# Kernel tuning notes

Hardware: AMD Instinct MI355X
Metric: run time of the kernel (lower is better)

The kernel has to match this reference:

```python
import jax, jax.numpy as jnp
import numpy as np

D_MODEL = 1024
N_HEADS = 16
D_K = 64
B = 2
S = 2048


def setup_inputs() -> dict:
    key = jax.random.key(0)
    ks = jax.random.split(key, 6)
    scale = 1.0 / np.sqrt(D_MODEL)
    x = jax.random.normal(ks[0], (B, S, D_MODEL), dtype=jnp.float32)
    Wq = jax.random.normal(ks[1], (D_MODEL, D_MODEL), dtype=jnp.float32) * scale
    Wk = jax.random.normal(ks[2], (D_MODEL, D_MODEL), dtype=jnp.float32) * scale
    Wv = jax.random.normal(ks[3], (D_MODEL, D_MODEL), dtype=jnp.float32) * scale
    Wo = jax.random.normal(ks[4], (D_MODEL, D_MODEL), dtype=jnp.float32) * scale
    bq = jnp.zeros((D_MODEL,), jnp.float32)
    bk = jnp.zeros((D_MODEL,), jnp.float32)
    bv = jnp.zeros((D_MODEL,), jnp.float32)
    bo = jnp.zeros((D_MODEL,), jnp.float32)
    # causal mask, broadcast over batch and heads: [1, 1, S, S]
    mask = jnp.tril(jnp.ones((S, S), jnp.int32))[None, None, :, :]
    return {"x": x, "mask": mask, "Wq": Wq, "bq": bq, "Wk": Wk, "bk": bk,
            "Wv": Wv, "bv": bv, "Wo": Wo, "bo": bo}


def reference(x, mask, Wq, bq, Wk, bk, Wv, bv, Wo, bo):
    b, s, _ = x.shape
    # projections (torch Linear: y = x @ W^T + b); split heads -> [b, h, s, d_k]
    def split_heads(y):
        return y.reshape(b, s, N_HEADS, D_K).transpose(0, 2, 1, 3)
    Q = split_heads(x @ Wq.T + bq)
    K = split_heads(x @ Wk.T + bk)
    V = split_heads(x @ Wv.T + bv)
    scores = jnp.einsum('bhqd,bhkd->bhqk', Q, K) / jnp.sqrt(jnp.float32(D_K))
    scores = jnp.where(mask == 0, -jnp.inf, scores)
    attn = jax.nn.softmax(scores, axis=-1)  # dropout p=0 -> identity
    out = jnp.einsum('bhqk,bhkd->bhqd', attn, V)
    out = out.transpose(0, 2, 1, 3).reshape(b, s, D_MODEL)
    return out @ Wo.T + bo
```

## Files before the change

### kernel.cpp

```cpp
#include <hip/hip_runtime.h>
#include <math.h>
#include <type_traits>

#define D_MODEL 1024
#define N_HEADS 16
#define D_KK    64
#define B_SZ    2
#define SEQ     2048
#define M_TOTAL (B_SZ * SEQ)

#define QSCALE 0.18033688011112042f
#define FIXM 12.0f

typedef __attribute__((ext_vector_type(8)))  short short8;
typedef __attribute__((ext_vector_type(4)))  float f32x4;
typedef __attribute__((ext_vector_type(16))) float f32x16;

static __device__ __forceinline__ ushort f2bf(float f) {
    union { float f; unsigned u; } c; c.f = f;
    unsigned u = c.u;
    unsigned r = (u + 0x7fffu + ((u >> 16) & 1u)) >> 16;
    return (ushort)r;
}

static __device__ __forceinline__ unsigned cvtpk(float a, float b) {
    unsigned r;
    asm("v_cvt_pk_bf16_f32 %0, %1, %2" : "=v"(r) : "v"(a), "v"(b));
    return r;
}
static __device__ __forceinline__ void pswap(unsigned &a, unsigned &b) {
    asm("v_permlane32_swap_b32 %0, %1" : "+v"(a), "+v"(b));
}

static __device__ __forceinline__ void gload16(const void* g, void* l) {
    __builtin_amdgcn_global_load_lds(
        (const __attribute__((address_space(1))) void*)g,
        (__attribute__((address_space(3))) void*)l, 16, 0, 0);
}

__global__ __launch_bounds__(256)
void cvt_kernel(const float* __restrict__ x,  const float* __restrict__ wq,
                const float* __restrict__ wk, const float* __restrict__ wv,
                const float* __restrict__ wo,
                ushort* __restrict__ xb,  ushort* __restrict__ wqb,
                ushort* __restrict__ wkb, ushort* __restrict__ wvb,
                ushort* __restrict__ wob)
{
    const float* s; ushort* d; int n4;
    switch (blockIdx.y) {
        case 0:  s = x;  d = xb;  n4 = M_TOTAL * D_MODEL / 4; break;
        case 1:  s = wq; d = wqb; n4 = D_MODEL * D_MODEL / 4; break;
        case 2:  s = wk; d = wkb; n4 = D_MODEL * D_MODEL / 4; break;
        case 3:  s = wv; d = wvb; n4 = D_MODEL * D_MODEL / 4; break;
        default: s = wo; d = wob; n4 = D_MODEL * D_MODEL / 4; break;
    }
    const int stride = gridDim.x * blockDim.x;
    for (int i = blockIdx.x * blockDim.x + threadIdx.x; i < n4; i += stride) {
        float4 v = reinterpret_cast<const float4*>(s)[i];
        ushort4 u;
        u.x = f2bf(v.x); u.y = f2bf(v.y); u.z = f2bf(v.z); u.w = f2bf(v.w);
        reinterpret_cast<ushort4*>(d)[i] = u;
    }
}

template<int EPI>
__global__ __launch_bounds__(256)
void gemm_mfma(const ushort* __restrict__ A,
               const ushort* __restrict__ W0, const float* __restrict__ b0, void* __restrict__ C0,
               const ushort* __restrict__ W1, const float* __restrict__ b1, void* __restrict__ C1,
               const ushort* __restrict__ W2, const float* __restrict__ b2, void* __restrict__ C2)
{
    constexpr int K = D_MODEL;

    __shared__ ushort As[2][128 * 64];
    __shared__ ushort Bs[2][64 * 64];

    const int id  = blockIdx.x;
    const int xcd = id & 7;
    const int j   = id >> 3;
    const int mt  = xcd * 4 + (j & 3);
    const int ntz = j >> 2;
    const int nt  = ntz & 15;
    const int z   = ntz >> 4;

    const ushort* W    = W0;
    const float*  bias = b0;
    void*         C    = C0;
    if (z == 1) { W = W1; bias = b1; C = C1; }
    else if (z == 2) { W = W2; bias = b2; C = C2; }

    const int m0 = mt * 128;
    const int n0 = nt * 64;

    const int tid  = threadIdx.x;
    const int w    = tid >> 6;
    const int lane = tid & 63;
    const int lr   = lane & 15;
    const int lc   = lane >> 4;
    const int wr   = w >> 1;
    const int wc   = w & 1;

    const int rsub = lane >> 3;
    const int csw  = ((lane & 7) ^ rsub) << 3;

    const ushort* gA = A + (size_t)(m0 + w * 8 + rsub) * K + csw;
    const ushort* gB = W + (size_t)(n0 + w * 8 + rsub) * K + csw;

    f32x4 acc[4][2];
#pragma unroll
    for (int m = 0; m < 4; ++m)
#pragma unroll
        for (int n = 0; n < 2; ++n) acc[m][n] = (f32x4)0.0f;

#pragma unroll
    for (int ca = 0; ca < 4; ++ca)
        gload16(gA + (size_t)(32 * ca) * K, &As[0][(w + 4 * ca) * 512]);
#pragma unroll
    for (int cb = 0; cb < 2; ++cb)
        gload16(gB + (size_t)(32 * cb) * K, &Bs[0][(w + 4 * cb) * 512]);
    __syncthreads();

    const int swz = (lr & 7) << 4;
    int buf = 0;
    for (int it = 0; it < 16; ++it) {
        if (it < 15) {
            const int kn = (it + 1) * 64;
#pragma unroll
            for (int ca = 0; ca < 4; ++ca)
                gload16(gA + (size_t)(32 * ca) * K + kn, &As[buf ^ 1][(w + 4 * ca) * 512]);
#pragma unroll
            for (int cb = 0; cb < 2; ++cb)
                gload16(gB + (size_t)(32 * cb) * K + kn, &Bs[buf ^ 1][(w + 4 * cb) * 512]);
        }

        short8 af[4][2], bfr[2][2];
#pragma unroll
        for (int m = 0; m < 4; ++m) {
            const int rbyte = (wr * 64 + m * 16 + lr) * 128;
#pragma unroll
            for (int kk = 0; kk < 2; ++kk)
                af[m][kk] = *reinterpret_cast<const short8*>(
                    &As[buf][(rbyte + ((kk * 64 + lc * 16) ^ swz)) >> 1]);
        }
#pragma unroll
        for (int n = 0; n < 2; ++n) {
            const int rbyte = (wc * 32 + n * 16 + lr) * 128;
#pragma unroll
            for (int kk = 0; kk < 2; ++kk)
                bfr[n][kk] = *reinterpret_cast<const short8*>(
                    &Bs[buf][(rbyte + ((kk * 64 + lc * 16) ^ swz)) >> 1]);
        }
#pragma unroll
        for (int kk = 0; kk < 2; ++kk)
#pragma unroll
            for (int m = 0; m < 4; ++m)
#pragma unroll
                for (int n = 0; n < 2; ++n)
                    acc[m][n] = __builtin_amdgcn_mfma_f32_16x16x32_bf16(
                        af[m][kk], bfr[n][kk], acc[m][n], 0, 0, 0);

        __syncthreads();
        buf ^= 1;
    }

    float bv[2];
#pragma unroll
    for (int n = 0; n < 2; ++n) bv[n] = bias[n0 + wc * 32 + n * 16 + lr];
    const int row_base = m0 + wr * 64;

    if (EPI == 0) {
        float* Cf = (float*)C;
#pragma unroll
        for (int m = 0; m < 4; ++m)
#pragma unroll
        for (int r = 0; r < 4; ++r) {
            const int row = row_base + m * 16 + lc * 4 + r;
#pragma unroll
            for (int n = 0; n < 2; ++n)
                Cf[(size_t)row * D_MODEL + n0 + wc * 32 + n * 16 + lr] =
                    acc[m][n][r] + bv[n];
        }
    } else {
        ushort* Cu = (ushort*)C;
        const bool vt   = (z == 2);
        const float osc = (z == 0) ? QSCALE : 1.0f;
#pragma unroll
        for (int m = 0; m < 4; ++m) {
            const int row4 = row_base + m * 16 + lc * 4;
            const int bb = row4 >> 11;
            const int ss = row4 & 2047;
            const size_t bhbase = (size_t)bb * N_HEADS;
#pragma unroll
            for (int n = 0; n < 2; ++n) {
                const int col = n0 + wc * 32 + n * 16 + lr;
                const int h = col >> 6, d = col & 63;
                if (vt) {
                    ushort4 u;
                    u.x = f2bf(acc[m][n][0] + bv[n]);
                    u.y = f2bf(acc[m][n][1] + bv[n]);
                    u.z = f2bf(acc[m][n][2] + bv[n]);
                    u.w = f2bf(acc[m][n][3] + bv[n]);
                    *reinterpret_cast<ushort4*>(
                        &Cu[((bhbase + h) * D_KK + d) * SEQ + ss]) = u;
                } else {
#pragma unroll
                    for (int r = 0; r < 4; ++r)
                        Cu[((bhbase + h) * SEQ + ss + r) * D_KK + d] =
                            f2bf((acc[m][n][r] + bv[n]) * osc);
                }
            }
        }
    }
}

__global__ __launch_bounds__(128)
void attn_mfma_kernel(const ushort* __restrict__ Qb, const ushort* __restrict__ Kb,
                      const ushort* __restrict__ Vt, ushort* __restrict__ Ob)
{
    __shared__ ushort Ks[2][4096];
    __shared__ ushort Vs[2][4096];

    const int tid  = threadIdx.x;
    const int w    = tid >> 6;
    const int lane = tid & 63;
    const int l31  = lane & 31;
    const int hi   = lane >> 5;
    const int swl  = (lane & 7) << 4;

    const int id  = blockIdx.x;
    const int xcd = id & 7;
    const int j   = id >> 3;
    const int bh  = xcd * 4 + (j & 3);
    const int qx  = j >> 2;
    const int b   = bh >> 4;
    const int h   = bh & 15;

    const ushort* Kbase = Kb + (size_t)bh * SEQ * D_KK;
    const ushort* Vbase = Vt + (size_t)bh * D_KK * SEQ;

    const int rsub = lane >> 3;
    const int csw  = ((lane & 7) ^ rsub) << 3;

    auto stage = [&](int kofs, int s) {
#pragma unroll
        for (int cc = 0; cc < 4; ++cc) {
            const int c = w + cc * 2;
            gload16(Kbase + (size_t)(kofs + c * 8 + rsub) * D_KK + csw,
                    &Ks[s][c * 512]);
            gload16(Vbase + (size_t)(c * 8 + rsub) * SEQ + kofs + csw,
                    &Vs[s][c * 512]);
        }
    };

    auto makefrag = [&](const f32x16& sv, int o) -> short8 {
        unsigned u0 = cvtpk(sv[o + 0], sv[o + 1]);
        unsigned u1 = cvtpk(sv[o + 2], sv[o + 3]);
        unsigned u2 = cvtpk(sv[o + 4], sv[o + 5]);
        unsigned u3 = cvtpk(sv[o + 6], sv[o + 7]);
        pswap(u0, u2);
        pswap(u1, u3);
        int4 t = make_int4((int)u0, (int)u1, (int)u2, (int)u3);
        return *reinterpret_cast<short8*>(&t);
    };

    const int qrel = 32 * w + l31;

    for (int half = 0; half < 2; ++half) {
        const int qb  = half ? (31 - qx) : qx;
        const int q0  = qb * 64;
        const int qw0 = q0 + w * 32;
        const int nt  = qb + 1;

        const ushort* Qp = Qb + ((size_t)bh * SEQ + qw0 + l31) * D_KK + 8 * hi;
        short8 qf[4];
#pragma unroll
        for (int ds = 0; ds < 4; ++ds)
            qf[ds] = *reinterpret_cast<const short8*>(Qp + 16 * ds);

        f32x16 ot0 = (f32x16)0.0f, ot1 = (f32x16)0.0f;
        float l_run = 0.0f;

        stage(0, 0);
        __syncthreads();

        auto tile_body = [&](int buf, auto maskc) {
            constexpr bool MASK = decltype(maskc)::value;
            const ushort* Ksb = &Ks[buf][0];
            const ushort* Vsb = &Vs[buf][0];

            f32x16 s0 = (f32x16)0.0f, s1 = (f32x16)0.0f;
#pragma unroll
            for (int ds = 0; ds < 4; ++ds) {
                const int cb = (32 * ds + 16 * hi) ^ swl;
                const short8 a0 = *reinterpret_cast<const short8*>(
                    &Ksb[(l31 * 128 + cb) >> 1]);
                const short8 a1 = *reinterpret_cast<const short8*>(
                    &Ksb[((32 + l31) * 128 + cb) >> 1]);
                s0 = __builtin_amdgcn_mfma_f32_32x32x16_bf16(a0, qf[ds], s0, 0, 0, 0);
                s1 = __builtin_amdgcn_mfma_f32_32x32x16_bf16(a1, qf[ds], s1, 0, 0, 0);
            }

            if (MASK) {
#pragma unroll
                for (int reg = 0; reg < 16; ++reg) {
                    const int k32 = (reg & 3) + 8 * (reg >> 2) + 4 * hi;
                    if (k32 > qrel)      s0[reg] = -1e30f;
                    if (k32 + 32 > qrel) s1[reg] = -1e30f;
                }
            }

            float rsum = 0.0f;
#pragma unroll
            for (int reg = 0; reg < 16; ++reg) {
                const float p0 = __builtin_amdgcn_exp2f(s0[reg] - FIXM);
                const float p1 = __builtin_amdgcn_exp2f(s1[reg] - FIXM);
                s0[reg] = p0; s1[reg] = p1;
                rsum += p0 + p1;
            }
            l_run += rsum;

            const short8 pb0 = makefrag(s0, 0);
            const short8 pb1 = makefrag(s0, 8);
            const short8 pb2 = makefrag(s1, 0);
            const short8 pb3 = makefrag(s1, 8);

#pragma unroll
            for (int dg = 0; dg < 2; ++dg) {
                const int row = dg * 32 + l31;
                f32x16& ot = dg ? ot1 : ot0;
#pragma unroll
                for (int ks = 0; ks < 4; ++ks) {
                    const int cb = (32 * ks + 16 * hi) ^ swl;
                    const short8 vf = *reinterpret_cast<const short8*>(
                        &Vsb[(row * 128 + cb) >> 1]);
                    const short8 pb = (ks == 0) ? pb0 : (ks == 1) ? pb1
                                     : (ks == 2) ? pb2 : pb3;
                    ot = __builtin_amdgcn_mfma_f32_32x32x16_bf16(vf, pb, ot, 0, 0, 0);
                }
            }
        };

        int buf = 0;
        for (int it = 0; it < nt; ++it) {
            if (it + 1 < nt) stage((it + 1) * 64, buf ^ 1);
            if (it == nt - 1)
                tile_body(buf, std::integral_constant<bool, true>{});
            else
                tile_body(buf, std::integral_constant<bool, false>{});
            __syncthreads();
            buf ^= 1;
        }

        const float l_tot = l_run + __shfl_xor(l_run, 32);
        const float linv  = 1.0f / l_tot;
        ushort* Op = Ob + ((size_t)b * SEQ + qw0 + l31) * D_MODEL + h * D_KK;
#pragma unroll
        for (int dg = 0; dg < 2; ++dg) {
            const f32x16& ot = dg ? ot1 : ot0;
#pragma unroll
            for (int m = 0; m < 4; ++m) {
                ushort4 u;
                u.x = f2bf(ot[4 * m + 0] * linv);
                u.y = f2bf(ot[4 * m + 1] * linv);
                u.z = f2bf(ot[4 * m + 2] * linv);
                u.w = f2bf(ot[4 * m + 3] * linv);
                *reinterpret_cast<ushort4*>(&Op[dg * 32 + m * 8 + 4 * hi]) = u;
            }
        }
    }
}

extern "C" void kernel_launch(void* const* d_in, const int* in_sizes, int n_in,
                              void* d_out, int out_size, void* d_ws, size_t ws_size,
                              hipStream_t stream)
{
    const float* x  = (const float*)d_in[0];
    const float* Wq = (const float*)d_in[2];
    const float* bq = (const float*)d_in[3];
    const float* Wk = (const float*)d_in[4];
    const float* bk = (const float*)d_in[5];
    const float* Wv = (const float*)d_in[6];
    const float* bv = (const float*)d_in[7];
    const float* Wo = (const float*)d_in[8];
    const float* bo = (const float*)d_in[9];
    float* out = (float*)d_out;

    const size_t TSZ = (size_t)M_TOTAL * D_MODEL;
    const size_t WSZ = (size_t)D_MODEL * D_MODEL;
    ushort* xb  = (ushort*)d_ws;
    ushort* Wqb = xb  + TSZ;
    ushort* Wkb = Wqb + WSZ;
    ushort* Wvb = Wkb + WSZ;
    ushort* Wob = Wvb + WSZ;
    ushort* Qb  = Wob + WSZ;
    ushort* Kb  = Qb  + TSZ;
    ushort* Vt  = Kb  + TSZ;
    ushort* Ob  = Vt  + TSZ;

    dim3 blk(256);
    cvt_kernel<<<dim3(256, 5), blk, 0, stream>>>(x, Wq, Wk, Wv, Wo,
                                                 xb, Wqb, Wkb, Wvb, Wob);

    gemm_mfma<1><<<dim3(1536), blk, 0, stream>>>(xb, Wqb, bq, Qb,
                                                     Wkb, bk, Kb,
                                                     Wvb, bv, Vt);

    attn_mfma_kernel<<<dim3(512), dim3(128), 0, stream>>>(Qb, Kb, Vt, Ob);

    gemm_mfma<0><<<dim3(512), blk, 0, stream>>>(Ob, Wob, bo, out,
                                                    Wob, bo, out,
                                                    Wob, bo, out);
}
```

Baseline: 120.8 us.

## Process both causal query halves concurrently in 4-wave attention blocks sharing K/V tiles

```diff
diff --git a/kernel.cpp b/kernel.cpp
--- a/kernel.cpp
+++ b/kernel.cpp
@@ -213,7 +213,7 @@
     }
 }
 
-__global__ __launch_bounds__(128)
+__global__ __launch_bounds__(256, 2)
 void attn_mfma_kernel(const ushort* __restrict__ Qb, const ushort* __restrict__ Kb,
                       const ushort* __restrict__ Vt, ushort* __restrict__ Ob)
 {
@@ -235,6 +235,11 @@
     const int b   = bh >> 4;
     const int h   = bh & 15;
 
+    const int myqb = (w < 2) ? qx : (31 - qx);
+    const int qw0  = myqb * 64 + (w & 1) * 32;
+    const int qr   = (w & 1) * 32 + l31;
+    const int ntmx = 32 - qx;
+
     const ushort* Kbase = Kb + (size_t)bh * SEQ * D_KK;
     const ushort* Vbase = Vt + (size_t)bh * D_KK * SEQ;
 
@@ -243,8 +248,8 @@
 
     auto stage = [&](int kofs, int s) {
 #pragma unroll
-        for (int cc = 0; cc < 4; ++cc) {
-            const int c = w + cc * 2;
+        for (int cc = 0; cc < 2; ++cc) {
+            const int c = w + cc * 4;
             gload16(Kbase + (size_t)(kofs + c * 8 + rsub) * D_KK + csw,
                     &Ks[s][c * 512]);
             gload16(Vbase + (size_t)(c * 8 + rsub) * SEQ + kofs + csw,
@@ -263,28 +268,23 @@
         return *reinterpret_cast<short8*>(&t);
     };
 
-    const int qrel = 32 * w + l31;
-
-    for (int half = 0; half < 2; ++half) {
-        const int qb  = half ? (31 - qx) : qx;
-        const int q0  = qb * 64;
-        const int qw0 = q0 + w * 32;
-        const int nt  = qb + 1;
-
-        const ushort* Qp = Qb + ((size_t)bh * SEQ + qw0 + l31) * D_KK + 8 * hi;
-        short8 qf[4];
-#pragma unroll
-        for (int ds = 0; ds < 4; ++ds)
-            qf[ds] = *reinterpret_cast<const short8*>(Qp + 16 * ds);
-
-        f32x16 ot0 = (f32x16)0.0f, ot1 = (f32x16)0.0f;
-        float l_run = 0.0f;
-
-        stage(0, 0);
-        __syncthreads();
-
-        auto tile_body = [&](int buf, auto maskc) {
-            constexpr bool MASK = decltype(maskc)::value;
+    const ushort* Qp = Qb + ((size_t)bh * SEQ + qw0 + l31) * D_KK + 8 * hi;
+    short8 qf[4];
+#pragma unroll
+    for (int ds = 0; ds < 4; ++ds)
+        qf[ds] = *reinterpret_cast<const short8*>(Qp + 16 * ds);
+
+    f32x16 ot0 = (f32x16)0.0f, ot1 = (f32x16)0.0f;
+    float l_run = 0.0f;
+
+    stage(0, 0);
+    __syncthreads();
+
+    int buf = 0;
+    for (int it = 0; it < ntmx; ++it) {
+        if (it + 1 < ntmx) stage((it + 1) * 64, buf ^ 1);
+
+        if (it <= myqb) {
             const ushort* Ksb = &Ks[buf][0];
             const ushort* Vsb = &Vs[buf][0];
 
@@ -300,12 +300,12 @@
                 s1 = __builtin_amdgcn_mfma_f32_32x32x16_bf16(a1, qf[ds], s1, 0, 0, 0);
             }
 
-            if (MASK) {
+            if (it == myqb) {
 #pragma unroll
                 for (int reg = 0; reg < 16; ++reg) {
                     const int k32 = (reg & 3) + 8 * (reg >> 2) + 4 * hi;
-                    if (k32 > qrel)      s0[reg] = -1e30f;
-                    if (k32 + 32 > qrel) s1[reg] = -1e30f;
+                    if (k32 > qr)      s0[reg] = -1e30f;
+                    if (k32 + 32 > qr) s1[reg] = -1e30f;
                 }
             }
 
@@ -338,34 +338,26 @@
                     ot = __builtin_amdgcn_mfma_f32_32x32x16_bf16(vf, pb, ot, 0, 0, 0);
                 }
             }
-        };
-
-        int buf = 0;
-        for (int it = 0; it < nt; ++it) {
-            if (it + 1 < nt) stage((it + 1) * 64, buf ^ 1);
-            if (it == nt - 1)
-                tile_body(buf, std::integral_constant<bool, true>{});
-            else
-                tile_body(buf, std::integral_constant<bool, false>{});
-            __syncthreads();
-            buf ^= 1;
-        }
-
-        const float l_tot = l_run + __shfl_xor(l_run, 32);
-        const float linv  = 1.0f / l_tot;
-        ushort* Op = Ob + ((size_t)b * SEQ + qw0 + l31) * D_MODEL + h * D_KK;
-#pragma unroll
-        for (int dg = 0; dg < 2; ++dg) {
-            const f32x16& ot = dg ? ot1 : ot0;
-#pragma unroll
-            for (int m = 0; m < 4; ++m) {
-                ushort4 u;
-                u.x = f2bf(ot[4 * m + 0] * linv);
-                u.y = f2bf(ot[4 * m + 1] * linv);
-                u.z = f2bf(ot[4 * m + 2] * linv);
-                u.w = f2bf(ot[4 * m + 3] * linv);
-                *reinterpret_cast<ushort4*>(&Op[dg * 32 + m * 8 + 4 * hi]) = u;
-            }
+        }
+
+        __syncthreads();
+        buf ^= 1;
+    }
+
+    const float l_tot = l_run + __shfl_xor(l_run, 32);
+    const float linv  = 1.0f / l_tot;
+    ushort* Op = Ob + ((size_t)b * SEQ + qw0 + l31) * D_MODEL + h * D_KK;
+#pragma unroll
+    for (int dg = 0; dg < 2; ++dg) {
+        const f32x16& ot = dg ? ot1 : ot0;
+#pragma unroll
+        for (int m = 0; m < 4; ++m) {
+            ushort4 u;
+            u.x = f2bf(ot[4 * m + 0] * linv);
+            u.y = f2bf(ot[4 * m + 1] * linv);
+            u.z = f2bf(ot[4 * m + 2] * linv);
+            u.w = f2bf(ot[4 * m + 3] * linv);
+            *reinterpret_cast<ushort4*>(&Op[dg * 32 + m * 8 + 4 * hi]) = u;
         }
     }
 }
@@ -405,7 +397,7 @@
                                                      Wkb, bk, Kb,
                                                      Wvb, bv, Vt);
 
-    attn_mfma_kernel<<<dim3(512), dim3(128), 0, stream>>>(Qb, Kb, Vt, Ob);
+    attn_mfma_kernel<<<dim3(512), blk, 0, stream>>>(Qb, Kb, Vt, Ob);
 
     gemm_mfma<0><<<dim3(512), blk, 0, stream>>>(Ob, Wob, bo, out,
                                                     Wob, bo, out,
```

After: 107.2 us. 1.13x faster.
